# Kernel optimization log

Hardware: AMD Instinct MI355X
Metric: run time of the kernel (lower is better)

The kernel has to match this reference:

```python
import jax, jax.numpy as jnp
import numpy as np

# Sizes from init_kwargs / input_specs
D_MODEL = 1024; D_INT = 64; KW = 32; B = 2; L = 4096
SAMPLING = np.array([5, 5, 2, 1, 1]); DILATIONS = np.array([1, 1, 2, 4, 8])
SUBHEADS = len(SAMPLING); HEADS = int(SAMPLING.sum())  # 5, 14
HEAD_OF_SUB = np.repeat(np.arange(SUBHEADS), SAMPLING)  # subhead index for each head
HEAD_DIL = np.repeat(DILATIONS, SAMPLING)                # dilation for each head


def _win_idx(dil):
    # centered dilated band, clipped at sequence edges -> [L, KW]
    offs = (np.arange(KW) - KW // 2) * dil
    return np.clip(np.arange(L)[:, None] + offs[None, :], 0, L - 1)

SUB_IDX = jnp.asarray(np.stack([_win_idx(d) for d in DILATIONS]))  # [SUBHEADS, L, KW]
HEAD_IDX = jnp.asarray(np.stack([_win_idx(d) for d in HEAD_DIL]))  # [HEADS, L, KW]


def setup_inputs() -> dict:
    rng = jax.random.key(0)
    ks = jax.random.split(rng, 9)
    n = lambda i, sh, sc=1.0: jax.random.normal(ks[i], sh, dtype=jnp.float32) * sc
    return dict(
        query=n(0, (B, L, D_MODEL)),
        key=n(1, (B, L, D_MODEL)),
        value=n(2, (B, L, D_MODEL)),
        Wq=n(3, (SUBHEADS, D_MODEL, D_INT), 0.02),
        bq=jnp.zeros((SUBHEADS, D_INT), jnp.float32),
        Wk=n(4, (SUBHEADS, D_MODEL, D_INT), 0.02),
        bk=jnp.zeros((SUBHEADS, D_INT), jnp.float32),
        Wv=n(5, (HEADS, D_MODEL, D_INT), 0.02),
        bv=jnp.zeros((HEADS, D_INT), jnp.float32),
        Ws=n(6, (HEADS, KW, KW), 0.05) + jnp.eye(KW, dtype=jnp.float32)[None],
        bs=jnp.zeros((HEADS, KW), jnp.float32),
        Wc=n(7, (HEADS * D_INT, D_MODEL), 0.02),
        bc=jnp.zeros((D_MODEL,), jnp.float32),
    )


def reference(query, key, value, Wq, bq, Wk, bk, Wv, bv, Ws, bs, Wc, bc):
    # per-subhead query/key projections: [S, B, L, Di]
    q = jnp.einsum('bld,sdi->sbli', query, Wq) + bq[:, None, None, :]
    k = jnp.einsum('bld,sdi->sbli', key, Wk) + bk[:, None, None, :]
    # per-head value projection: [H, B, L, Di]
    v = jnp.einsum('bld,hdi->hbli', value, Wv) + bv[:, None, None, :]
    # dilated banded key windows per subhead: [S, B, L, KW, Di]
    kw = jax.vmap(lambda kh, ix: kh[:, ix], in_axes=(0, 0))(k, SUB_IDX)
    # banded scores [S, B, L, KW]
    scores = jnp.einsum('sbli,sblki->sblk', q, kw) / jnp.sqrt(jnp.float32(D_INT))
    # supersample: replicate each subhead's scores to its heads -> [H, B, L, KW]
    scores_h = scores[HEAD_OF_SUB]
    # per-head positional supersampling linear on the score window
    sampled = jnp.einsum('hblk,hkm->hblm', scores_h, Ws) + bs[:, None, None, :]
    attn = jax.nn.softmax(sampled, axis=-1)
    # dilated value windows per head: [H, B, L, KW, Di]
    vw = jax.vmap(lambda vh, ix: vh[:, ix], in_axes=(0, 0))(v, HEAD_IDX)
    out = jnp.einsum('hblk,hblki->hbli', attn, vw)  # [H, B, L, Di]
    out = jnp.transpose(out, (1, 2, 0, 3)).reshape(B, L, HEADS * D_INT)
    return out @ Wc + bc  # [B, L, D_MODEL]
```

## Files before the change

### kernel.cpp

```cpp
#include <hip/hip_runtime.h>
#include <math.h>

#define D_MODEL 1024
#define D_INT   64
#define KW      32
#define L_SEQ   4096
#define SUBHEADS 5
#define HEADS   14
#define M_ROWS  8192
#define N_CAT   896
#define NQK     320

typedef unsigned short us;
typedef unsigned int   uu;
typedef __attribute__((ext_vector_type(4))) unsigned int uu4;
typedef __attribute__((ext_vector_type(8))) short bf16x8_t;
typedef __attribute__((ext_vector_type(4))) float f32x4_t;

__device__ __forceinline__ float u2f(uu u) {
    float f; __builtin_memcpy(&f, &u, 4); return f;
}
__device__ __forceinline__ float blo(uu u) { return u2f(u << 16); }
__device__ __forceinline__ float bhi(uu u) { return u2f(u & 0xffff0000u); }
__device__ __forceinline__ us f2b(float f) {
    uu u; __builtin_memcpy(&u, &f, 4);
    u += 0x7fffu + ((u >> 16) & 1u);
    return (us)(u >> 16);
}
__device__ __forceinline__ uu pack2(float a, float b) {
    return (uu)f2b(a) | ((uu)f2b(b) << 16);
}
__device__ __forceinline__ void load16(void* lds, const void* g) {
    __builtin_amdgcn_global_load_lds(
        (const __attribute__((address_space(1))) unsigned int*)g,
        (__attribute__((address_space(3))) unsigned int*)lds, 16, 0, 0);
}
__device__ __forceinline__ int subhead_of(int h) {
    return (h < 5) ? 0 : (h < 10) ? 1 : (h < 12) ? 2 : (h == 12) ? 3 : 4;
}
__device__ __forceinline__ int dil_of_sub(int s) {
    return (s <= 1) ? 1 : (1 << (s - 1));
}

#define CAST_BLK 24576
__global__ __launch_bounds__(256)
void prep_kernel(const float4* __restrict__ q, const float4* __restrict__ k,
                 const float4* __restrict__ v,
                 const float* __restrict__ Wq, const float* __restrict__ Wk,
                 const float* __restrict__ Wv, const float* __restrict__ Wc,
                 us* __restrict__ Xq, us* __restrict__ Xk, us* __restrict__ Xv,
                 us* __restrict__ Wqt, us* __restrict__ Wkt,
                 us* __restrict__ Wvt, us* __restrict__ Wct)
{
    __shared__ float t[32][33];
    const int b = blockIdx.x, tid = threadIdx.x;

    if (b < CAST_BLK) {
        const int which = b >> 13;
        const int i = ((b & 8191) << 8) + tid;
        const float4* s = (which == 0) ? q : (which == 1) ? k : v;
        us* d = (which == 0) ? Xq : (which == 1) ? Xk : Xv;
        float4 x = s[i];
        ushort4 o;
        o.x = f2b(x.x); o.y = f2b(x.y); o.z = f2b(x.z); o.w = f2b(x.w);
        ((ushort4*)d)[i] = o;
        return;
    }

    int g = b - CAST_BLK;
    const float* S; us* D; int K, N;
    if (g < 640) {
        if (g < 320) { S = Wq; D = Wqt; } else { S = Wk; D = Wkt; g -= 320; }
        K = 1024; N = 64;
    } else if (g < 1536) {
        g -= 640; S = Wv; D = Wvt; K = 1024; N = 64;
    } else {
        g -= 1536; S = Wc; D = Wct; K = 896; N = 1024;
    }
    const int nkx = K >> 5;
    const int kx = g % nkx;
    const int rest = g / nkx;
    const int ny = rest % (N >> 5);
    const int z  = rest / (N >> 5);
    const int k0 = kx * 32, n0 = ny * 32;
    S += (size_t)z * K * N;
    D += (size_t)z * K * N;
    const int tx = tid & 31, ty = tid >> 5;
#pragma unroll
    for (int r = 0; r < 32; r += 8)
        t[r + ty][tx] = S[(size_t)(k0 + r + ty) * N + n0 + tx];
    __syncthreads();
#pragma unroll
    for (int r = 0; r < 32; r += 8)
        D[(size_t)(n0 + r + ty) * K + k0 + tx] = f2b(t[tx][r + ty]);
}

__device__ __forceinline__
void gemm64_core(const us* __restrict__ A, const us* __restrict__ Bt,
                 const float* __restrict__ bias, us* __restrict__ C,
                 int K, int ldC, us* As, us* Bs)
{
    const int row0 = blockIdx.x << 7, col0 = blockIdx.y << 6;
    const int tid = threadIdx.x, w = tid >> 6, lane = tid & 63;
    const int m = lane & 15, quad = lane >> 4;
    const int sr = lane >> 3;
    const int scs = (lane & 7) ^ sr;

    f32x4_t z4 = {0.f, 0.f, 0.f, 0.f};
    f32x4_t acc[2][4] = {{z4, z4, z4, z4}, {z4, z4, z4, z4}};

    for (int k0 = 0; k0 < K; k0 += 64) {
#pragma unroll
        for (int p = 0; p < 4; p++) {
            const int r = w * 32 + p * 8 + sr;
            load16(&As[(w * 32 + p * 8) * 64], A + (size_t)(row0 + r) * K + k0 + scs * 8);
        }
#pragma unroll
        for (int p = 0; p < 2; p++) {
            const int r = w * 16 + p * 8 + sr;
            load16(&Bs[(w * 16 + p * 8) * 64], Bt + (size_t)(col0 + r) * K + k0 + scs * 8);
        }
        __syncthreads();
#pragma unroll
        for (int ks = 0; ks < 2; ks++) {
            const int slot = ((ks * 4 + quad) ^ (m & 7)) * 8;
            bf16x8_t a0 = *(const bf16x8_t*)&As[(w * 32 + m) * 64 + slot];
            bf16x8_t a1 = *(const bf16x8_t*)&As[(w * 32 + 16 + m) * 64 + slot];
#pragma unroll
            for (int t = 0; t < 4; t++) {
                bf16x8_t bb = *(const bf16x8_t*)&Bs[(t * 16 + m) * 64 + slot];
                acc[0][t] = __builtin_amdgcn_mfma_f32_16x16x32_bf16(a0, bb, acc[0][t], 0, 0, 0);
                acc[1][t] = __builtin_amdgcn_mfma_f32_16x16x32_bf16(a1, bb, acc[1][t], 0, 0, 0);
            }
        }
        __syncthreads();
    }

#pragma unroll
    for (int tm = 0; tm < 2; tm++) {
        const int rbase = row0 + w * 32 + tm * 16 + quad * 4;
#pragma unroll
        for (int t = 0; t < 4; t++) {
            const int col = col0 + t * 16 + m;
            const float bi = bias[col];
#pragma unroll
            for (int r = 0; r < 4; r++)
                C[(size_t)(rbase + r) * ldC + col] = f2b(acc[tm][t][r] + bi);
        }
    }
}

__global__ __launch_bounds__(256)
void gemm_qk(const us* __restrict__ Xq, const us* __restrict__ Xk,
             const us* __restrict__ Wqt, const us* __restrict__ Wkt,
             const float* __restrict__ bq, const float* __restrict__ bk,
             us* __restrict__ qbuf, us* __restrict__ kbuf)
{
    __shared__ us As[128 * 64];
    __shared__ us Bs[64 * 64];
    const int z = blockIdx.z;
    gemm64_core(z ? Xk : Xq, z ? Wkt : Wqt, z ? bk : bq, z ? kbuf : qbuf,
                D_MODEL, NQK, As, Bs);
}

__global__ __launch_bounds__(256)
void gemm_bf16_128(const us* __restrict__ A, const us* __restrict__ Bt,
                   const float* __restrict__ bias, void* __restrict__ Cv,
                   int K, int ldC, int outBf16)
{
    __shared__ us As[128 * 64];
    __shared__ us Bs[128 * 64];
    const int row0 = blockIdx.x << 7, col0 = blockIdx.y << 7;
    const int tid = threadIdx.x, w = tid >> 6, lane = tid & 63;
    const int m = lane & 15, quad = lane >> 4;
    const int sr = lane >> 3;
    const int scs = (lane & 7) ^ sr;
    const int mrow0 = (w & 1) * 64, ncol0 = (w >> 1) * 64;

    f32x4_t z = {0.f, 0.f, 0.f, 0.f};
    f32x4_t acc[4][4] = {{z,z,z,z},{z,z,z,z},{z,z,z,z},{z,z,z,z}};

    for (int k0 = 0; k0 < K; k0 += 64) {
#pragma unroll
        for (int p = 0; p < 4; p++) {
            const int r = w * 32 + p * 8 + sr;
            load16(&As[(w * 32 + p * 8) * 64], A  + (size_t)(row0 + r) * K + k0 + scs * 8);
            load16(&Bs[(w * 32 + p * 8) * 64], Bt + (size_t)(col0 + r) * K + k0 + scs * 8);
        }
        __syncthreads();
#pragma unroll
        for (int ks = 0; ks < 2; ks++) {
            const int slot = ((ks * 4 + quad) ^ (m & 7)) * 8;
            bf16x8_t a[4], b[4];
#pragma unroll
            for (int t = 0; t < 4; t++) {
                a[t] = *(const bf16x8_t*)&As[(mrow0 + t * 16 + m) * 64 + slot];
                b[t] = *(const bf16x8_t*)&Bs[(ncol0 + t * 16 + m) * 64 + slot];
            }
#pragma unroll
            for (int i = 0; i < 4; i++)
#pragma unroll
                for (int j = 0; j < 4; j++)
                    acc[i][j] = __builtin_amdgcn_mfma_f32_16x16x32_bf16(a[i], b[j], acc[i][j], 0, 0, 0);
        }
        __syncthreads();
    }

#pragma unroll
    for (int i = 0; i < 4; i++) {
        const int rbase = row0 + mrow0 + i * 16 + quad * 4;
        if (outBf16) {
            us* Cb = (us*)Cv;
#pragma unroll
            for (int j = 0; j < 4; j++) {
                const int col = col0 + ncol0 + j * 16 + m;
                const float bi = bias[col];
#pragma unroll
                for (int r = 0; r < 4; r++)
                    Cb[(size_t)(rbase + r) * ldC + col] = f2b(acc[i][j][r] + bi);
            }
        } else {
            float* Cb = (float*)Cv;
#pragma unroll
            for (int j = 0; j < 4; j++) {
                const int col = col0 + ncol0 + j * 16 + m;
                const float bi = bias[col];
#pragma unroll
                for (int r = 0; r < 4; r++)
                    Cb[(size_t)(rbase + r) * ldC + col] = acc[i][j][r] + bi;
            }
        }
    }
}

template<int ROWS>
__global__ __launch_bounds__(256)
void score_kernel(const us* __restrict__ qb, const us* __restrict__ kb,
                  float* __restrict__ scores, int sbase)
{
    __shared__ uu kslab[ROWS * 36];
    __shared__ uu qslab[64 * 32];

    const int tid  = threadIdx.x;
    const int wave = tid >> 6;
    const int lane = tid & 63;
    const int j    = lane & 31;
    const int half = lane >> 5;
    const int s    = sbase + blockIdx.y;
    const int d    = dil_of_sub(s);
    const int ml0  = blockIdx.x * 64;
    const int l0   = ml0 & 4095;
    const int bm   = ml0 - l0;
    const int W    = 64 + 31 * d;

    const uu* kg = (const uu*)kb;
    const uu* qg = (const uu*)qb;

    for (int idx = tid; idx < W * 32; idx += 256) {
        int r = idx >> 5, c = idx & 31;
        int src = l0 - 16 * d + r;
        src = src < 0 ? 0 : (src > 4095 ? 4095 : src);
        kslab[r * 36 + c] = kg[(size_t)(bm + src) * 160 + s * 32 + c];
    }
    for (int idx = tid; idx < 64 * 32; idx += 256) {
        int r = idx >> 5, c = idx & 31;
        qslab[r * 32 + c] = qg[(size_t)(ml0 + r) * 160 + s * 32 + c];
    }
    __syncthreads();

#pragma unroll
    for (int i = 0; i < 8; i++) {
        const int p = wave * 16 + i * 2 + half;
        const uu4* k4 = (const uu4*)&kslab[(p + j * d) * 36];
        const uu4* q4 = (const uu4*)&qslab[p * 32];
        float acc = 0.f;
#pragma unroll
        for (int q = 0; q < 8; q++) {
            uu4 kd = k4[q];
            uu4 qd = q4[q];
            acc = fmaf(blo(kd.x), blo(qd.x), acc); acc = fmaf(bhi(kd.x), bhi(qd.x), acc);
            acc = fmaf(blo(kd.y), blo(qd.y), acc); acc = fmaf(bhi(kd.y), bhi(qd.y), acc);
            acc = fmaf(blo(kd.z), blo(qd.z), acc); acc = fmaf(bhi(kd.z), bhi(qd.z), acc);
            acc = fmaf(blo(kd.w), blo(qd.w), acc); acc = fmaf(bhi(kd.w), bhi(qd.w), acc);
        }
        scores[((size_t)s * M_ROWS + ml0 + p) * 32 + j] = acc * 0.125f;
    }
}

template<int ROWS>
__global__ __launch_bounds__(256)
void head_kernel(const float* __restrict__ scores, const us* __restrict__ vb,
                 const float* __restrict__ Ws, const float* __restrict__ bs,
                 us* __restrict__ ab, int hbase)
{
    __shared__ uu    vslab[ROWS * 36];
    __shared__ float sab[64 * 36];

    const int tid  = threadIdx.x;
    const int wave = tid >> 6;
    const int lane = tid & 63;
    const int j    = lane & 31;
    const int half = lane >> 5;
    const int h    = hbase + blockIdx.y;
    const int s    = subhead_of(h);
    const int d    = dil_of_sub(s);
    const int ml0  = blockIdx.x * 64;
    const int l0   = ml0 & 4095;
    const int bm   = ml0 - l0;
    const int W    = 64 + 31 * d;

    const uu* vg = (const uu*)vb;
    for (int idx = tid; idx < W * 32; idx += 256) {
        int r = idx >> 5, c = idx & 31;
        int src = l0 - 16 * d + r;
        src = src < 0 ? 0 : (src > 4095 ? 4095 : src);
        vslab[r * 36 + c] = vg[(size_t)(bm + src) * 448 + h * 32 + c];
    }
    {
        const float4* g4 = (const float4*)(scores + ((size_t)s * M_ROWS + ml0) * 32);
#pragma unroll
        for (int t = 0; t < 2; t++) {
            int i4 = t * 256 + tid;
            int r = i4 >> 3, c4 = i4 & 7;
            *(float4*)&sab[r * 36 + c4 * 4] = g4[i4];
        }
    }
    float wsr[32];
#pragma unroll
    for (int k = 0; k < 32; k++) wsr[k] = Ws[(size_t)h * 1024 + k * 32 + j];
    const float bsv = bs[h * 32 + j];
    __syncthreads();

#pragma unroll
    for (int i = 0; i < 8; i++) {
        const int p = wave * 16 + i * 2 + half;
        const float4* s4 = (const float4*)&sab[p * 36];
        float acc = bsv;
#pragma unroll
        for (int q = 0; q < 8; q++) {
            float4 v = s4[q];
            acc = fmaf(v.x, wsr[q * 4 + 0], acc);
            acc = fmaf(v.y, wsr[q * 4 + 1], acc);
            acc = fmaf(v.z, wsr[q * 4 + 2], acc);
            acc = fmaf(v.w, wsr[q * 4 + 3], acc);
        }
        float mx = acc;
#pragma unroll
        for (int off = 16; off > 0; off >>= 1) mx = fmaxf(mx, __shfl_xor(mx, off, 64));
        float ex = __expf(acc - mx);
        float sum = ex;
#pragma unroll
        for (int off = 16; off > 0; off >>= 1) sum += __shfl_xor(sum, off, 64);
        sab[p * 36 + j] = ex / sum;
    }

    const int o = lane >> 3;
    const int c = lane & 7;
#pragma unroll
    for (int pass = 0; pass < 2; pass++) {
        const int p  = wave * 16 + pass * 8 + o;
        const int ml = ml0 + p;
        float a0 = 0.f, a1 = 0.f, a2 = 0.f, a3 = 0.f;
        float a4 = 0.f, a5 = 0.f, a6 = 0.f, a7 = 0.f;
#pragma unroll
        for (int mm = 0; mm < 32; mm++) {
            const float at = sab[p * 36 + mm];
            uu4 vd = *(const uu4*)&vslab[(p + mm * d) * 36 + c * 4];
            a0 = fmaf(blo(vd.x), at, a0); a1 = fmaf(bhi(vd.x), at, a1);
            a2 = fmaf(blo(vd.y), at, a2); a3 = fmaf(bhi(vd.y), at, a3);
            a4 = fmaf(blo(vd.z), at, a4); a5 = fmaf(bhi(vd.z), at, a5);
            a6 = fmaf(blo(vd.w), at, a6); a7 = fmaf(bhi(vd.w), at, a7);
        }
        uu4 od;
        od.x = pack2(a0, a1); od.y = pack2(a2, a3);
        od.z = pack2(a4, a5); od.w = pack2(a6, a7);
        *(uu4*)&((uu*)ab)[(size_t)ml * 448 + h * 32 + c * 4] = od;
    }
}

extern "C" void kernel_launch(void* const* d_in, const int* in_sizes, int n_in,
                              void* d_out, int out_size, void* d_ws, size_t ws_size,
                              hipStream_t stream)
{
    const float* query = (const float*)d_in[0];
    const float* key   = (const float*)d_in[1];
    const float* value = (const float*)d_in[2];
    const float* Wq    = (const float*)d_in[3];
    const float* bq    = (const float*)d_in[4];
    const float* Wk    = (const float*)d_in[5];
    const float* bk    = (const float*)d_in[6];
    const float* Wv    = (const float*)d_in[7];
    const float* bv    = (const float*)d_in[8];
    const float* Ws    = (const float*)d_in[9];
    const float* bs    = (const float*)d_in[10];
    const float* Wc    = (const float*)d_in[11];
    const float* bc    = (const float*)d_in[12];
    float* out = (float*)d_out;

    us* w = (us*)d_ws;
    us* Xq  = w;
    us* ab  = w;
    us* Xk  = Xq  + (size_t)M_ROWS * D_MODEL;
    float* scores = (float*)Xk;
    us* Xv  = Xk  + (size_t)M_ROWS * D_MODEL;
    us* Wqt = Xv  + (size_t)M_ROWS * D_MODEL;
    us* Wkt = Wqt + (size_t)SUBHEADS * D_INT * D_MODEL;
    us* Wvt = Wkt + (size_t)SUBHEADS * D_INT * D_MODEL;
    us* Wct = Wvt + (size_t)HEADS * D_INT * D_MODEL;
    us* qbuf = Wct + (size_t)D_MODEL * N_CAT;
    us* kbuf = qbuf + (size_t)M_ROWS * NQK;
    us* vbuf = kbuf + (size_t)M_ROWS * NQK;

    dim3 blk(256);

    prep_kernel<<<dim3(CAST_BLK + 2432), blk, 0, stream>>>(
        (const float4*)query, (const float4*)key, (const float4*)value,
        Wq, Wk, Wv, Wc, Xq, Xk, Xv, Wqt, Wkt, Wvt, Wct);

    gemm_qk<<<dim3(M_ROWS / 128, NQK / 64, 2), blk, 0, stream>>>(
        Xq, Xk, Wqt, Wkt, bq, bk, qbuf, kbuf);

    gemm_bf16_128<<<dim3(M_ROWS / 128, N_CAT / 128), blk, 0, stream>>>(
        Xv, Wvt, bv, vbuf, D_MODEL, N_CAT, 1);

    score_kernel<126><<<dim3(M_ROWS / 64, 3), blk, 0, stream>>>(qbuf, kbuf, scores, 0);
    score_kernel<312><<<dim3(M_ROWS / 64, 2), blk, 0, stream>>>(qbuf, kbuf, scores, 3);

    head_kernel<312><<<dim3(M_ROWS / 64, 2),  blk, 0, stream>>>(scores, vbuf, Ws, bs, ab, 12);
    head_kernel<126><<<dim3(M_ROWS / 64, 12), blk, 0, stream>>>(scores, vbuf, Ws, bs, ab, 0);

    gemm_bf16_128<<<dim3(M_ROWS / 128, D_MODEL / 128), blk, 0, stream>>>(
        ab, Wct, bc, out, N_CAT, D_MODEL, 0);
}
```

Baseline: 284.2 us.

## Fuse fp32-to-bf16 input cast into projection GEMM loads and merge QKV launches

```diff
diff --git a/kernel.cpp b/kernel.cpp
--- a/kernel.cpp
+++ b/kernel.cpp
@@ -30,6 +30,11 @@
 __device__ __forceinline__ uu pack2(float a, float b) {
     return (uu)f2b(a) | ((uu)f2b(b) << 16);
 }
+__device__ __forceinline__ uu cvtpk(float a, float b) {
+    uu r;
+    asm("v_cvt_pk_bf16_f32 %0, %1, %2" : "=v"(r) : "v"(a), "v"(b));
+    return r;
+}
 __device__ __forceinline__ void load16(void* lds, const void* g) {
     __builtin_amdgcn_global_load_lds(
         (const __attribute__((address_space(1))) unsigned int*)g,
@@ -42,32 +47,15 @@
     return (s <= 1) ? 1 : (1 << (s - 1));
 }
 
-#define CAST_BLK 24576
 __global__ __launch_bounds__(256)
-void prep_kernel(const float4* __restrict__ q, const float4* __restrict__ k,
-                 const float4* __restrict__ v,
-                 const float* __restrict__ Wq, const float* __restrict__ Wk,
+void prep_kernel(const float* __restrict__ Wq, const float* __restrict__ Wk,
                  const float* __restrict__ Wv, const float* __restrict__ Wc,
-                 us* __restrict__ Xq, us* __restrict__ Xk, us* __restrict__ Xv,
                  us* __restrict__ Wqt, us* __restrict__ Wkt,
                  us* __restrict__ Wvt, us* __restrict__ Wct)
 {
     __shared__ float t[32][33];
-    const int b = blockIdx.x, tid = threadIdx.x;
-
-    if (b < CAST_BLK) {
-        const int which = b >> 13;
-        const int i = ((b & 8191) << 8) + tid;
-        const float4* s = (which == 0) ? q : (which == 1) ? k : v;
-        us* d = (which == 0) ? Xq : (which == 1) ? Xk : Xv;
-        float4 x = s[i];
-        ushort4 o;
-        o.x = f2b(x.x); o.y = f2b(x.y); o.z = f2b(x.z); o.w = f2b(x.w);
-        ((ushort4*)d)[i] = o;
-        return;
-    }
-
-    int g = b - CAST_BLK;
+    const int tid = threadIdx.x;
+    int g = blockIdx.x;
     const float* S; us* D; int K, N;
     if (g < 640) {
         if (g < 320) { S = Wq; D = Wqt; } else { S = Wk; D = Wkt; g -= 320; }
@@ -95,12 +83,12 @@
         D[(size_t)(n0 + r + ty) * K + k0 + tx] = f2b(t[tx][r + ty]);
 }
 
+template<bool AF32>
 __device__ __forceinline__
-void gemm64_core(const us* __restrict__ A, const us* __restrict__ Bt,
+void gemm64_core(const void* __restrict__ Av, const us* __restrict__ Bt,
                  const float* __restrict__ bias, us* __restrict__ C,
-                 int K, int ldC, us* As, us* Bs)
-{
-    const int row0 = blockIdx.x << 7, col0 = blockIdx.y << 6;
+                 int K, int ldC, int row0, int col0, us* As, us* Bs)
+{
     const int tid = threadIdx.x, w = tid >> 6, lane = tid & 63;
     const int m = lane & 15, quad = lane >> 4;
     const int sr = lane >> 3;
@@ -111,14 +99,25 @@
 
     for (int k0 = 0; k0 < K; k0 += 64) {
 #pragma unroll
-        for (int p = 0; p < 4; p++) {
-            const int r = w * 32 + p * 8 + sr;
-            load16(&As[(w * 32 + p * 8) * 64], A + (size_t)(row0 + r) * K + k0 + scs * 8);
-        }
-#pragma unroll
         for (int p = 0; p < 2; p++) {
             const int r = w * 16 + p * 8 + sr;
             load16(&Bs[(w * 16 + p * 8) * 64], Bt + (size_t)(col0 + r) * K + k0 + scs * 8);
+        }
+#pragma unroll
+        for (int p = 0; p < 4; p++) {
+            const int r = w * 32 + p * 8 + sr;
+            if constexpr (AF32) {
+                const float* ag = (const float*)Av + (size_t)(row0 + r) * K + k0 + scs * 8;
+                float4 x0 = *(const float4*)ag;
+                float4 x1 = *(const float4*)(ag + 4);
+                uu4 o;
+                o.x = cvtpk(x0.x, x0.y); o.y = cvtpk(x0.z, x0.w);
+                o.z = cvtpk(x1.x, x1.y); o.w = cvtpk(x1.z, x1.w);
+                *(uu4*)&As[(w * 32 + p * 8 + sr) * 64 + (lane & 7) * 8] = o;
+            } else {
+                load16(&As[(w * 32 + p * 8) * 64],
+                       (const us*)Av + (size_t)(row0 + r) * K + k0 + scs * 8);
+            }
         }
         __syncthreads();
 #pragma unroll
@@ -150,27 +149,13 @@
     }
 }
 
-__global__ __launch_bounds__(256)
-void gemm_qk(const us* __restrict__ Xq, const us* __restrict__ Xk,
-             const us* __restrict__ Wqt, const us* __restrict__ Wkt,
-             const float* __restrict__ bq, const float* __restrict__ bk,
-             us* __restrict__ qbuf, us* __restrict__ kbuf)
-{
-    __shared__ us As[128 * 64];
-    __shared__ us Bs[64 * 64];
-    const int z = blockIdx.z;
-    gemm64_core(z ? Xk : Xq, z ? Wkt : Wqt, z ? bk : bq, z ? kbuf : qbuf,
-                D_MODEL, NQK, As, Bs);
-}
-
-__global__ __launch_bounds__(256)
-void gemm_bf16_128(const us* __restrict__ A, const us* __restrict__ Bt,
-                   const float* __restrict__ bias, void* __restrict__ Cv,
-                   int K, int ldC, int outBf16)
-{
-    __shared__ us As[128 * 64];
-    __shared__ us Bs[128 * 64];
-    const int row0 = blockIdx.x << 7, col0 = blockIdx.y << 7;
+template<bool AF32>
+__device__ __forceinline__
+void gemm128_core(const void* __restrict__ Av, const us* __restrict__ Bt,
+                  const float* __restrict__ bias, void* __restrict__ Cv,
+                  int K, int ldC, int outBf16, int row0, int col0,
+                  us* As, us* Bs)
+{
     const int tid = threadIdx.x, w = tid >> 6, lane = tid & 63;
     const int m = lane & 15, quad = lane >> 4;
     const int sr = lane >> 3;
@@ -184,8 +169,19 @@
 #pragma unroll
         for (int p = 0; p < 4; p++) {
             const int r = w * 32 + p * 8 + sr;
-            load16(&As[(w * 32 + p * 8) * 64], A  + (size_t)(row0 + r) * K + k0 + scs * 8);
             load16(&Bs[(w * 32 + p * 8) * 64], Bt + (size_t)(col0 + r) * K + k0 + scs * 8);
+            if constexpr (AF32) {
+                const float* ag = (const float*)Av + (size_t)(row0 + r) * K + k0 + scs * 8;
+                float4 x0 = *(const float4*)ag;
+                float4 x1 = *(const float4*)(ag + 4);
+                uu4 o;
+                o.x = cvtpk(x0.x, x0.y); o.y = cvtpk(x0.z, x0.w);
+                o.z = cvtpk(x1.x, x1.y); o.w = cvtpk(x1.z, x1.w);
+                *(uu4*)&As[(w * 32 + p * 8 + sr) * 64 + (lane & 7) * 8] = o;
+            } else {
+                load16(&As[(w * 32 + p * 8) * 64],
+                       (const us*)Av + (size_t)(row0 + r) * K + k0 + scs * 8);
+            }
         }
         __syncthreads();
 #pragma unroll
@@ -231,6 +227,45 @@
             }
         }
     }
+}
+
+__global__ __launch_bounds__(256)
+void proj_kernel(const float* __restrict__ q, const float* __restrict__ k,
+                 const float* __restrict__ v,
+                 const us* __restrict__ Wqt, const us* __restrict__ Wkt,
+                 const us* __restrict__ Wvt,
+                 const float* __restrict__ bq, const float* __restrict__ bk,
+                 const float* __restrict__ bv,
+                 us* __restrict__ qbuf, us* __restrict__ kbuf,
+                 us* __restrict__ vbuf)
+{
+    __shared__ us As[128 * 64];
+    __shared__ us Bs[128 * 64];
+    const int b = blockIdx.x;
+    if (b < 448) {
+        const int bx = b & 63, cy = b >> 6;
+        gemm128_core<true>(v, Wvt, bv, vbuf, D_MODEL, N_CAT, 1,
+                           bx << 7, cy << 7, As, Bs);
+    } else {
+        const int idx = b - 448;
+        const int bx = idx & 63;
+        const int rest = idx >> 6;
+        const int cy = rest % 5, z = rest / 5;
+        gemm64_core<true>(z ? (const void*)k : (const void*)q,
+                          z ? Wkt : Wqt, z ? bk : bq,
+                          z ? kbuf : qbuf, D_MODEL, NQK,
+                          bx << 7, cy << 6, As, Bs);
+    }
+}
+
+__global__ __launch_bounds__(256)
+void gemm_out(const us* __restrict__ ab, const us* __restrict__ Wct,
+              const float* __restrict__ bc, float* __restrict__ out)
+{
+    __shared__ us As[128 * 64];
+    __shared__ us Bs[128 * 64];
+    gemm128_core<false>(ab, Wct, bc, out, N_CAT, D_MODEL, 0,
+                        (int)(blockIdx.x << 7), (int)(blockIdx.y << 7), As, Bs);
 }
 
 template<int ROWS>
@@ -413,15 +448,11 @@
 
     dim3 blk(256);
 
-    prep_kernel<<<dim3(CAST_BLK + 2432), blk, 0, stream>>>(
-        (const float4*)query, (const float4*)key, (const float4*)value,
-        Wq, Wk, Wv, Wc, Xq, Xk, Xv, Wqt, Wkt, Wvt, Wct);
-
-    gemm_qk<<<dim3(M_ROWS / 128, NQK / 64, 2), blk, 0, stream>>>(
-        Xq, Xk, Wqt, Wkt, bq, bk, qbuf, kbuf);
-
-    gemm_bf16_128<<<dim3(M_ROWS / 128, N_CAT / 128), blk, 0, stream>>>(
-        Xv, Wvt, bv, vbuf, D_MODEL, N_CAT, 1);
+    prep_kernel<<<dim3(2432), blk, 0, stream>>>(
+        Wq, Wk, Wv, Wc, Wqt, Wkt, Wvt, Wct);
+
+    proj_kernel<<<dim3(1088), blk, 0, stream>>>(
+        query, key, value, Wqt, Wkt, Wvt, bq, bk, bv, qbuf, kbuf, vbuf);
 
     score_kernel<126><<<dim3(M_ROWS / 64, 3), blk, 0, stream>>>(qbuf, kbuf, scores, 0);
     score_kernel<312><<<dim3(M_ROWS / 64, 2), blk, 0, stream>>>(qbuf, kbuf, scores, 3);
@@ -429,6 +460,6 @@
     head_kernel<312><<<dim3(M_ROWS / 64, 2),  blk, 0, stream>>>(scores, vbuf, Ws, bs, ab, 12);
     head_kernel<126><<<dim3(M_ROWS / 64, 12), blk, 0, stream>>>(scores, vbuf, Ws, bs, ab, 0);
 
-    gemm_bf16_128<<<dim3(M_ROWS / 128, D_MODEL / 128), blk, 0, stream>>>(
-        ab, Wct, bc, out, N_CAT, D_MODEL, 0);
-}
+    gemm_out<<<dim3(M_ROWS / 128, D_MODEL / 128), blk, 0, stream>>>(
+        ab, Wct, bc, out);
+}
```

New measurement: 288.7 us. Within noise of the previous version (+1.6%).
